# Optimization experiments

Hardware: AMD Instinct MI355X
Metric: run time of the kernel (lower is better)

The kernel has to match this reference:

```python
import jax, jax.numpy as jnp
import numpy as np

N_SPECIES = 1024
N_T1 = 20000
N_T2 = 60000
BATCH = 1024


def setup_inputs() -> dict:
    key = jax.random.key(0)
    ks = jax.random.split(key, 8)
    return {
        "t_in": jax.random.uniform(ks[0], (1,), dtype=jnp.float32),
        "y_in": jax.random.uniform(ks[1], (BATCH, N_SPECIES), dtype=jnp.float32),
        "rates_1st": jax.random.normal(ks[2], (N_T1,), dtype=jnp.float32),
        "rates_2nd": jax.random.normal(ks[3], (N_T2,), dtype=jnp.float32),
        "den_norm": jnp.ones((1,), dtype=jnp.float32),
        "inds_r1": jax.random.randint(ks[4], (N_T1,), 0, N_SPECIES),
        "inds_r2a": jax.random.randint(ks[5], (N_T2,), 0, N_SPECIES),
        "inds_r2b": jax.random.randint(ks[6], (N_T2,), 0, N_SPECIES),
        "inds_out1": jax.random.randint(ks[7], (N_T1,), 0, N_SPECIES),
        "inds_out2": jax.random.randint(jax.random.fold_in(key, 99), (N_T2,), 0, N_SPECIES),
    }


def reference(t_in, y_in, rates_1st, rates_2nd, den_norm,
              inds_r1, inds_r2a, inds_r2b, inds_out1, inds_out2):
    # t_in is unused by ConstantRateTerm (rates are constant in time).
    n = y_in.shape[-1]
    # 1st-order terms: signed_rate * y[reactant]  -> scatter-add to target species
    term1 = y_in[:, inds_r1] * rates_1st                      # (B, T1)
    out = jnp.zeros_like(y_in).at[:, inds_out1].add(term1)    # (B, N)
    # 2nd-order terms: den_norm * signed_rate * y[r1] * y[r2]
    term2 = (y_in[:, inds_r2a] * y_in[:, inds_r2b]) * (rates_2nd * den_norm[0])  # (B, T2)
    out = out.at[:, inds_out2].add(term2)
    return out
```

## Files before the change

kernel.cpp:

```cpp
#include <hip/hip_runtime.h>
#include <hip/hip_bf16.h>

#define NSP    1024
#define ROWS   4
#define BLK    256
#define QUARTS 4
#define MAXK   160

#define WS_COUNTS 0
#define WS_TERMS  8192

__global__ __launch_bounds__(256) void scatter_kernel(
    const int* __restrict__ r1, const int* __restrict__ o1,
    const float* __restrict__ rates1, int n1,
    const int* __restrict__ r2a, const int* __restrict__ r2b,
    const int* __restrict__ o2, const float* __restrict__ rates2, int n2,
    const float* __restrict__ den_ptr,
    int* __restrict__ counts, int2* __restrict__ terms_T)
{
    const float den = den_ptr[0];
    const int total = n1 + n2;
    int i = blockIdx.x * blockDim.x + threadIdx.x;
    int stride = gridDim.x * blockDim.x;

    for (int t = i; t < total; t += stride) {
        if (t < n1) {
            int s = o1[t];
            int pos = atomicAdd(&counts[NSP + s], 1);
            int slot = MAXK - 1 - pos;
            if (slot >= 0)
                terms_T[(size_t)slot * NSP + s] =
                    make_int2(r1[t], __float_as_int(rates1[t]));
        } else {
            int u = t - n1;
            int s = o2[u];
            int pos = atomicAdd(&counts[s], 1);
            if (pos < MAXK)
                terms_T[(size_t)pos * NSP + s] =
                    make_int2(r2a[u] | (r2b[u] << 16),
                              __float_as_int(rates2[u] * den));
        }
    }
}

__global__ __launch_bounds__(BLK) void gather_kernel(
    const float* __restrict__ y,
    const int* __restrict__ counts,
    const int2* __restrict__ terms_T,
    float* __restrict__ out)
{
    __shared__ float4 ys[NSP];

    const int tid   = threadIdx.x;
    const int rg    = blockIdx.x / QUARTS;
    const int quart = blockIdx.x % QUARTS;
    const int row0  = rg * ROWS;

    for (int i = tid; i < ROWS * NSP; i += BLK) {
        int r = i >> 10;
        int c = i & (NSP - 1);
        ((float*)&ys[c])[r] = y[(size_t)(row0 + r) * NSP + c];
    }
    __syncthreads();

    const int s  = quart * BLK + tid;
    const int c2 = counts[s];
    const int c1 = counts[NSP + s];

    float4 acc = make_float4(0.0f, 0.0f, 0.0f, 0.0f);

#pragma unroll 4
    for (int k = 0; k < c2; ++k) {
        const int2 e = terms_T[(size_t)k * NSP + s];
        const int a = e.x & 0xFFFF;
        const int b = e.x >> 16;
        const float w = __int_as_float(e.y);
        const float4 ya = ys[a];
        const float4 yb = ys[b];
        acc.x += w * ya.x * yb.x;
        acc.y += w * ya.y * yb.y;
        acc.z += w * ya.z * yb.z;
        acc.w += w * ya.w * yb.w;
    }

#pragma unroll 4
    for (int q = 0; q < c1; ++q) {
        const int2 e = terms_T[(size_t)(MAXK - 1 - q) * NSP + s];
        const float w = __int_as_float(e.y);
        const float4 ya = ys[e.x];
        acc.x += w * ya.x;
        acc.y += w * ya.y;
        acc.z += w * ya.z;
        acc.w += w * ya.w;
    }

    out[(size_t)(row0 + 0) * NSP + s] = acc.x;
    out[(size_t)(row0 + 1) * NSP + s] = acc.y;
    out[(size_t)(row0 + 2) * NSP + s] = acc.z;
    out[(size_t)(row0 + 3) * NSP + s] = acc.w;
}

extern "C" void kernel_launch(void* const* d_in, const int* in_sizes, int n_in,
                              void* d_out, int out_size, void* d_ws, size_t ws_size,
                              hipStream_t stream) {
    const float* y      = (const float*)d_in[1];
    const float* rates1 = (const float*)d_in[2];
    const float* rates2 = (const float*)d_in[3];
    const float* den    = (const float*)d_in[4];
    const int* r1  = (const int*)d_in[5];
    const int* r2a = (const int*)d_in[6];
    const int* r2b = (const int*)d_in[7];
    const int* o1  = (const int*)d_in[8];
    const int* o2  = (const int*)d_in[9];
    float* out = (float*)d_out;

    const int n_t1  = in_sizes[2];
    const int n_t2  = in_sizes[3];
    const int batch = in_sizes[1] / NSP;

    char* ws = (char*)d_ws;
    int*  counts  = (int*)(ws + WS_COUNTS);
    int2* terms_T = (int2*)(ws + WS_TERMS);

    hipMemsetAsync(counts, 0, 2 * NSP * sizeof(int), stream);
    scatter_kernel<<<256, 256, 0, stream>>>(r1, o1, rates1, n_t1,
                                            r2a, r2b, o2, rates2, n_t2,
                                            den, counts, terms_T);
    gather_kernel<<<(batch / ROWS) * QUARTS, BLK, 0, stream>>>(y, counts, terms_T, out);
}
```

Measured before the change: 112.6 us.

## Bucket terms by reactant-minus-species residue to cut LDS bank conflicts

Result: slower. 123.1 us (+9.3%).

```diff
diff --git a/kernel.cpp b/kernel.cpp
--- a/kernel.cpp
+++ b/kernel.cpp
@@ -1,14 +1,16 @@
 #include <hip/hip_runtime.h>
-#include <hip/hip_bf16.h>
 
 #define NSP    1024
 #define ROWS   4
 #define BLK    256
 #define QUARTS 4
-#define MAXK   160
+#define CAP2   32
+#define CAP1   20
 
-#define WS_COUNTS 0
-#define WS_TERMS  8192
+#define WS_CNT2   0
+#define WS_CNT1   32768
+#define WS_TERMS2 65536
+#define WS_TERMS1 (65536 + 8 * CAP2 * NSP * 8)
 
 __global__ __launch_bounds__(256) void scatter_kernel(
     const int* __restrict__ r1, const int* __restrict__ o1,
@@ -16,37 +18,41 @@
     const int* __restrict__ r2a, const int* __restrict__ r2b,
     const int* __restrict__ o2, const float* __restrict__ rates2, int n2,
     const float* __restrict__ den_ptr,
-    int* __restrict__ counts, int2* __restrict__ terms_T)
+    int* __restrict__ cnt2, int* __restrict__ cnt1,
+    int2* __restrict__ terms2, int2* __restrict__ terms1)
 {
-    const float den = den_ptr[0];
     const int total = n1 + n2;
-    int i = blockIdx.x * blockDim.x + threadIdx.x;
-    int stride = gridDim.x * blockDim.x;
+    const int t = blockIdx.x * blockDim.x + threadIdx.x;
+    if (t >= total) return;
 
-    for (int t = i; t < total; t += stride) {
-        if (t < n1) {
-            int s = o1[t];
-            int pos = atomicAdd(&counts[NSP + s], 1);
-            int slot = MAXK - 1 - pos;
-            if (slot >= 0)
-                terms_T[(size_t)slot * NSP + s] =
-                    make_int2(r1[t], __float_as_int(rates1[t]));
-        } else {
-            int u = t - n1;
-            int s = o2[u];
-            int pos = atomicAdd(&counts[s], 1);
-            if (pos < MAXK)
-                terms_T[(size_t)pos * NSP + s] =
-                    make_int2(r2a[u] | (r2b[u] << 16),
-                              __float_as_int(rates2[u] * den));
-        }
+    if (t < n1) {
+        const int s = o1[t];
+        const int a = r1[t];
+        const int q = ((a & 7) - (s & 7)) & 7;
+        const int pos = atomicAdd(&cnt1[s * 8 + q], 1);
+        if (pos < CAP1)
+            terms1[(size_t)(q * CAP1 + pos) * NSP + s] =
+                make_int2(a, __float_as_int(rates1[t]));
+    } else {
+        const int u = t - n1;
+        const int s = o2[u];
+        const int a = r2a[u];
+        const int b = r2b[u];
+        const int q = ((a & 7) - (s & 7)) & 7;
+        const int pos = atomicAdd(&cnt2[s * 8 + q], 1);
+        if (pos < CAP2)
+            terms2[(size_t)(q * CAP2 + pos) * NSP + s] =
+                make_int2(a | (b << 16),
+                          __float_as_int(rates2[u] * den_ptr[0]));
     }
 }
 
 __global__ __launch_bounds__(BLK) void gather_kernel(
     const float* __restrict__ y,
-    const int* __restrict__ counts,
-    const int2* __restrict__ terms_T,
+    const int* __restrict__ cnt2,
+    const int* __restrict__ cnt1,
+    const int2* __restrict__ terms2,
+    const int2* __restrict__ terms1,
     float* __restrict__ out)
 {
     __shared__ float4 ys[NSP];
@@ -56,42 +62,64 @@
     const int quart = blockIdx.x % QUARTS;
     const int row0  = rg * ROWS;
 
-    for (int i = tid; i < ROWS * NSP; i += BLK) {
-        int r = i >> 10;
-        int c = i & (NSP - 1);
-        ((float*)&ys[c])[r] = y[(size_t)(row0 + r) * NSP + c];
+    const float4* y4 = (const float4*)(y + (size_t)row0 * NSP);
+    for (int i = tid; i < ROWS * (NSP / 4); i += BLK) {
+        const int r  = i >> 8;
+        const int c4 = i & 255;
+        const float4 v = y4[r * (NSP / 4) + c4];
+        ((float*)&ys[4 * c4 + 0])[r] = v.x;
+        ((float*)&ys[4 * c4 + 1])[r] = v.y;
+        ((float*)&ys[4 * c4 + 2])[r] = v.z;
+        ((float*)&ys[4 * c4 + 3])[r] = v.w;
     }
     __syncthreads();
 
-    const int s  = quart * BLK + tid;
-    const int c2 = counts[s];
-    const int c1 = counts[NSP + s];
+    const int s = quart * BLK + tid;
+
+    const int4* cv2 = (const int4*)(cnt2 + (size_t)s * 8);
+    const int4  c2a = cv2[0], c2b = cv2[1];
+    const int4* cv1 = (const int4*)(cnt1 + (size_t)s * 8);
+    const int4  c1a = cv1[0], c1b = cv1[1];
+    const int n2[8] = { min(c2a.x, CAP2), min(c2a.y, CAP2), min(c2a.z, CAP2), min(c2a.w, CAP2),
+                        min(c2b.x, CAP2), min(c2b.y, CAP2), min(c2b.z, CAP2), min(c2b.w, CAP2) };
+    const int n1[8] = { min(c1a.x, CAP1), min(c1a.y, CAP1), min(c1a.z, CAP1), min(c1a.w, CAP1),
+                        min(c1b.x, CAP1), min(c1b.y, CAP1), min(c1b.z, CAP1), min(c1b.w, CAP1) };
 
     float4 acc = make_float4(0.0f, 0.0f, 0.0f, 0.0f);
 
-#pragma unroll 4
-    for (int k = 0; k < c2; ++k) {
-        const int2 e = terms_T[(size_t)k * NSP + s];
-        const int a = e.x & 0xFFFF;
-        const int b = e.x >> 16;
-        const float w = __int_as_float(e.y);
-        const float4 ya = ys[a];
-        const float4 yb = ys[b];
-        acc.x += w * ya.x * yb.x;
-        acc.y += w * ya.y * yb.y;
-        acc.z += w * ya.z * yb.z;
-        acc.w += w * ya.w * yb.w;
+#pragma unroll
+    for (int Q = 0; Q < 8; ++Q) {
+        const int nn = n2[Q];
+        const int2* base = terms2 + (size_t)(Q * CAP2) * NSP + s;
+#pragma unroll 2
+        for (int k = 0; k < nn; ++k) {
+            const int2 e = base[(size_t)k * NSP];
+            const int a = e.x & 0xFFFF;
+            const int b = ((unsigned)e.x) >> 16;
+            const float w = __int_as_float(e.y);
+            const float4 ya = ys[a];
+            const float4 yb = ys[b];
+            acc.x += w * ya.x * yb.x;
+            acc.y += w * ya.y * yb.y;
+            acc.z += w * ya.z * yb.z;
+            acc.w += w * ya.w * yb.w;
+        }
     }
 
-#pragma unroll 4
-    for (int q = 0; q < c1; ++q) {
-        const int2 e = terms_T[(size_t)(MAXK - 1 - q) * NSP + s];
-        const float w = __int_as_float(e.y);
-        const float4 ya = ys[e.x];
-        acc.x += w * ya.x;
-        acc.y += w * ya.y;
-        acc.z += w * ya.z;
-        acc.w += w * ya.w;
+#pragma unroll
+    for (int Q = 0; Q < 8; ++Q) {
+        const int nn = n1[Q];
+        const int2* base = terms1 + (size_t)(Q * CAP1) * NSP + s;
+#pragma unroll 2
+        for (int k = 0; k < nn; ++k) {
+            const int2 e = base[(size_t)k * NSP];
+            const float w = __int_as_float(e.y);
+            const float4 ya = ys[e.x];
+            acc.x += w * ya.x;
+            acc.y += w * ya.y;
+            acc.z += w * ya.z;
+            acc.w += w * ya.w;
+        }
     }
 
     out[(size_t)(row0 + 0) * NSP + s] = acc.x;
@@ -119,12 +147,18 @@
     const int batch = in_sizes[1] / NSP;
 
     char* ws = (char*)d_ws;
-    int*  counts  = (int*)(ws + WS_COUNTS);
-    int2* terms_T = (int2*)(ws + WS_TERMS);
+    int*  cnt2   = (int*)(ws + WS_CNT2);
+    int*  cnt1   = (int*)(ws + WS_CNT1);
+    int2* terms2 = (int2*)(ws + WS_TERMS2);
+    int2* terms1 = (int2*)(ws + WS_TERMS1);
 
-    hipMemsetAsync(counts, 0, 2 * NSP * sizeof(int), stream);
-    scatter_kernel<<<256, 256, 0, stream>>>(r1, o1, rates1, n_t1,
-                                            r2a, r2b, o2, rates2, n_t2,
-                                            den, counts, terms_T);
-    gather_kernel<<<(batch / ROWS) * QUARTS, BLK, 0, stream>>>(y, counts, terms_T, out);
+    hipMemsetAsync(cnt2, 0, 2 * NSP * 8 * sizeof(int), stream);
+
+    const int total   = n_t1 + n_t2;
+    const int sblocks = (total + 255) / 256;
+    scatter_kernel<<<sblocks, 256, 0, stream>>>(r1, o1, rates1, n_t1,
+                                                r2a, r2b, o2, rates2, n_t2,
+                                                den, cnt2, cnt1, terms2, terms1);
+    gather_kernel<<<(batch / ROWS) * QUARTS, BLK, 0, stream>>>(y, cnt2, cnt1,
+                                                               terms2, terms1, out);
 }
```
